# Kernel tuning notes

Hardware: AMD Instinct MI355X
Metric: run time of the kernel (lower is better)

Reference implementation:

```python
import jax, jax.numpy as jnp
import numpy as np

B, V, T, K, N = 2048, 256, 11, 8, 8
H = 2 ** N - 1  # 255 combination neurons per slot


def setup_inputs() -> dict:
    key = jax.random.key(0)
    k0, k1, k2, k3, k4 = jax.random.split(key, 5)
    # one-hot character ids, matching make_scanner_batch semantics: (B, V, T, K)
    ids = jax.random.randint(k0, (B, T, K), 0, V)
    x_unfolded = jax.nn.one_hot(ids, V, axis=1, dtype=jnp.float32)
    # scanner_w ~ U(-1/sqrt(V), 1/sqrt(V)), shape (N, V, K)
    bv = 1.0 / np.sqrt(V).astype(np.float32)
    scanner_w = jax.random.uniform(k1, (N, V, K), jnp.float32, -bv, bv)
    # grouped 1x1 conv: torch weight (K*H, N, 1) -> store (K*H, N); fan_in = N
    bh = 1.0 / np.sqrt(N).astype(np.float32)
    hidden_w = jax.random.uniform(k2, (K * H, N), jnp.float32, -bh, bh)
    # output 1x1 conv: (2, K*H, 1) -> (2, K*H); fan_in = K*H
    bo = 1.0 / np.sqrt(K * H).astype(np.float32)
    out_w = jax.random.uniform(k3, (2, K * H), jnp.float32, -bo, bo)
    out_b = jax.random.uniform(k4, (2,), jnp.float32, -bo, bo)
    return {"x_unfolded": x_unfolded, "scanner_w": scanner_w,
            "hidden_w": hidden_w, "out_w": out_w, "out_b": out_b}


def reference(x_unfolded, scanner_w, hidden_w, out_w, out_b):
    # x_unfolded: (B, V, T, K); scanner_w: (N, V, K)
    b, v, t, k = x_unfolded.shape
    n = scanner_w.shape[0]
    h_per_slot = hidden_w.shape[0] // k
    # one-hot matmul (equivalent to a gather): result (B, K, N, T),
    # i.e. channel order after reshape is slot-major (k*N + n), matching
    # torch's permute(0,3,1,2).reshape(B, K*N, T).
    h = jax.nn.relu(jnp.einsum('bvtk,nvk->bknt', x_unfolded, scanner_w))
    # grouped 1x1 conv with groups=K: group k maps its N scanner values to
    # h_per_slot neurons. torch weight (K*H, N, 1) -> (K, H, N), where output
    # channel o belongs to group o // H.
    hw = hidden_w.reshape(k, h_per_slot, n)
    h2 = jax.nn.relu(jnp.einsum('bknt,khn->bkht', h, hw)).reshape(b, k * h_per_slot, t)
    # final 1x1 conv with bias: (B, 2, T)
    return jnp.einsum('bct,oc->bot', h2, out_w) + out_b[None, :, None]
```

## Files before the change

kernel.cpp:

```cpp
#include <hip/hip_runtime.h>

constexpr int B_ = 2048;
constexpr int V_ = 256;
constexpr int T_ = 11;
constexpr int K_ = 8;
constexpr int N_ = 8;
constexpr int H_ = 255;
constexpr int TK = T_ * K_;
constexpr int XB = V_ * TK;
constexpr int SLAB = 92;

__global__ __launch_bounds__(256, 3)
void scanner_fused(const float* __restrict__ x,
                   const float* __restrict__ sw,
                   const float* __restrict__ hw,
                   const float* __restrict__ ow,
                   const float* __restrict__ ob,
                   float* __restrict__ out)
{
    __shared__ int   ids_sh[TK];
    __shared__ float hsh[K_ * SLAB];
    __shared__ float wred[4][22];

    const int tid = threadIdx.x;
    const int b   = blockIdx.x;

    const float4* xb = (const float4*)(x + (size_t)b * XB);
    #pragma unroll
    for (int c = 0; c < 3; ++c) {
        const int nload = (c < 2) ? 8 : 6;
        float4 vbuf[8];
        #pragma unroll
        for (int i = 0; i < 8; ++i)
            if (i < nload) vbuf[i] = xb[(c * 8 + i) * 256 + tid];
        #pragma unroll
        for (int i = 0; i < 8; ++i) {
            if (i < nload) {
                const float4 q = vbuf[i];
                if ((q.x + q.y) + (q.z + q.w) != 0.0f) {
                    const int F = ((c * 8 + i) * 256 + tid) * 4;
                    if (q.x != 0.0f) { const int f = F;     const int v = f / TK; ids_sh[f - v * TK] = v; }
                    if (q.y != 0.0f) { const int f = F + 1; const int v = f / TK; ids_sh[f - v * TK] = v; }
                    if (q.z != 0.0f) { const int f = F + 2; const int v = f / TK; ids_sh[f - v * TK] = v; }
                    if (q.w != 0.0f) { const int f = F + 3; const int v = f / TK; ids_sh[f - v * TK] = v; }
                }
            }
        }
    }
    __syncthreads();

    #pragma unroll
    for (int j = 0; j < 3; ++j) {
        const int idx = j * 256 + tid;
        if (idx < TK * N_) {
            const int entry = idx >> 3;
            const int n     = idx & 7;
            const int t     = entry >> 3;
            const int k     = entry & 7;
            const int v     = ids_sh[entry];
            hsh[k * SLAB + t * 8 + n] = fmaxf(sw[(n * V_ + v) * K_ + k], 0.0f);
        }
    }
    __syncthreads();

    const int k2 = tid >> 5;
    const int hb = tid & 31;

    float hreg[T_][N_];
    #pragma unroll
    for (int t = 0; t < T_; ++t) {
        const float4* p = (const float4*)(hsh + k2 * SLAB + t * 8);
        const float4 a0 = p[0];
        const float4 a1 = p[1];
        hreg[t][0] = a0.x; hreg[t][1] = a0.y; hreg[t][2] = a0.z; hreg[t][3] = a0.w;
        hreg[t][4] = a1.x; hreg[t][5] = a1.y; hreg[t][6] = a1.z; hreg[t][7] = a1.w;
    }

    float acc0[T_], acc1[T_];
    #pragma unroll
    for (int t = 0; t < T_; ++t) { acc0[t] = 0.0f; acc1[t] = 0.0f; }

    #pragma unroll
    for (int i = 0; i < 8; ++i) {
        const int hh = hb + 32 * i;
        if (hh < H_) {
            const int row = k2 * H_ + hh;
            const float4* hwp = (const float4*)(hw + row * 8);
            const float4 w0 = hwp[0];
            const float4 w1 = hwp[1];
            const float o0 = ow[row];
            const float o1 = ow[K_ * H_ + row];
            #pragma unroll
            for (int t = 0; t < T_; ++t) {
                float pre = w0.x * hreg[t][0];
                pre = fmaf(w0.y, hreg[t][1], pre);
                pre = fmaf(w0.z, hreg[t][2], pre);
                pre = fmaf(w0.w, hreg[t][3], pre);
                pre = fmaf(w1.x, hreg[t][4], pre);
                pre = fmaf(w1.y, hreg[t][5], pre);
                pre = fmaf(w1.z, hreg[t][6], pre);
                pre = fmaf(w1.w, hreg[t][7], pre);
                const float h2 = fmaxf(pre, 0.0f);
                acc0[t] = fmaf(h2, o0, acc0[t]);
                acc1[t] = fmaf(h2, o1, acc1[t]);
            }
        }
    }

    #pragma unroll
    for (int t = 0; t < T_; ++t) {
        #pragma unroll
        for (int off = 32; off >= 1; off >>= 1) {
            acc0[t] += __shfl_xor(acc0[t], off, 64);
            acc1[t] += __shfl_xor(acc1[t], off, 64);
        }
    }
    const int wave = tid >> 6;
    const int lane = tid & 63;
    if (lane == 0) {
        #pragma unroll
        for (int t = 0; t < T_; ++t) {
            wred[wave][t]      = acc0[t];
            wred[wave][11 + t] = acc1[t];
        }
    }
    __syncthreads();

    if (tid < 22) {
        const float s = wred[0][tid] + wred[1][tid] + wred[2][tid] + wred[3][tid];
        out[(size_t)b * 22 + tid] = s + ob[tid / 11];
    }
}

extern "C" void kernel_launch(void* const* d_in, const int* in_sizes, int n_in,
                              void* d_out, int out_size, void* d_ws, size_t ws_size,
                              hipStream_t stream) {
    const float* x  = (const float*)d_in[0];
    const float* sw = (const float*)d_in[1];
    const float* hw = (const float*)d_in[2];
    const float* ow = (const float*)d_in[3];
    const float* ob = (const float*)d_in[4];
    float* out = (float*)d_out;

    scanner_fused<<<B_, 256, 0, stream>>>(x, sw, hw, ow, ob, out);
}
```

Before: 271.7 us.

## Split one-hot id scan into separate kernel feeding MLP kernel via workspace

Un-fuses the kernel. A bandwidth-bound scan kernel decodes the one-hot input into integer ids and writes them to workspace. A second compute kernel reads those ids and runs the scanner gather plus the two MLP layers. The aim is to let each phase run with occupancy suited to it (the scan kernel allows 4 blocks per SM) and to keep the 93 MB streaming read from competing with the FMA-heavy MLP. The costs are an extra launch, a global round trip for the ids, and the loss of overlap between memory and compute inside a single block.

```diff
diff --git a/kernel.cpp b/kernel.cpp
--- a/kernel.cpp
+++ b/kernel.cpp
@@ -10,13 +10,45 @@
 constexpr int XB = V_ * TK;
 constexpr int SLAB = 92;
 
+__global__ __launch_bounds__(256, 4)
+void scan_ids(const float* __restrict__ x,
+              int* __restrict__ ids)
+{
+    const int tid = threadIdx.x;
+    const int b   = blockIdx.x;
+    const uint4* xb = (const uint4*)(x + (size_t)b * XB);
+    int* __restrict__ idb = ids + b * TK;
+
+    #pragma unroll
+    for (int c = 0; c < 3; ++c) {
+        const int nload = (c < 2) ? 8 : 6;
+        uint4 vbuf[8];
+        #pragma unroll
+        for (int i = 0; i < 8; ++i)
+            if (i < nload) vbuf[i] = xb[(c * 8 + i) * 256 + tid];
+        #pragma unroll
+        for (int i = 0; i < 8; ++i) {
+            if (i < nload) {
+                const uint4 q = vbuf[i];
+                if (q.x | q.y | q.z | q.w) {
+                    const int F = ((c * 8 + i) * 256 + tid) * 4;
+                    if (q.x) { const int f = F;     const int v = f / TK; idb[f - v * TK] = v; }
+                    if (q.y) { const int f = F + 1; const int v = f / TK; idb[f - v * TK] = v; }
+                    if (q.z) { const int f = F + 2; const int v = f / TK; idb[f - v * TK] = v; }
+                    if (q.w) { const int f = F + 3; const int v = f / TK; idb[f - v * TK] = v; }
+                }
+            }
+        }
+    }
+}
+
 __global__ __launch_bounds__(256, 3)
-void scanner_fused(const float* __restrict__ x,
-                   const float* __restrict__ sw,
-                   const float* __restrict__ hw,
-                   const float* __restrict__ ow,
-                   const float* __restrict__ ob,
-                   float* __restrict__ out)
+void scanner_mlp(const int* __restrict__ ids,
+                 const float* __restrict__ sw,
+                 const float* __restrict__ hw,
+                 const float* __restrict__ ow,
+                 const float* __restrict__ ob,
+                 float* __restrict__ out)
 {
     __shared__ int   ids_sh[TK];
     __shared__ float hsh[K_ * SLAB];
@@ -25,28 +57,7 @@
     const int tid = threadIdx.x;
     const int b   = blockIdx.x;
 
-    const float4* xb = (const float4*)(x + (size_t)b * XB);
-    #pragma unroll
-    for (int c = 0; c < 3; ++c) {
-        const int nload = (c < 2) ? 8 : 6;
-        float4 vbuf[8];
-        #pragma unroll
-        for (int i = 0; i < 8; ++i)
-            if (i < nload) vbuf[i] = xb[(c * 8 + i) * 256 + tid];
-        #pragma unroll
-        for (int i = 0; i < 8; ++i) {
-            if (i < nload) {
-                const float4 q = vbuf[i];
-                if ((q.x + q.y) + (q.z + q.w) != 0.0f) {
-                    const int F = ((c * 8 + i) * 256 + tid) * 4;
-                    if (q.x != 0.0f) { const int f = F;     const int v = f / TK; ids_sh[f - v * TK] = v; }
-                    if (q.y != 0.0f) { const int f = F + 1; const int v = f / TK; ids_sh[f - v * TK] = v; }
-                    if (q.z != 0.0f) { const int f = F + 2; const int v = f / TK; ids_sh[f - v * TK] = v; }
-                    if (q.w != 0.0f) { const int f = F + 3; const int v = f / TK; ids_sh[f - v * TK] = v; }
-                }
-            }
-        }
-    }
+    if (tid < TK) ids_sh[tid] = ids[b * TK + tid];
     __syncthreads();
 
     #pragma unroll
@@ -142,5 +153,8 @@
     const float* ob = (const float*)d_in[4];
     float* out = (float*)d_out;
 
-    scanner_fused<<<B_, 256, 0, stream>>>(x, sw, hw, ow, ob, out);
+    int* ids = (int*)d_ws;
+
+    scan_ids<<<B_, 256, 0, stream>>>(x, ids);
+    scanner_mlp<<<B_, 256, 0, stream>>>(ids, sw, hw, ow, ob, out);
 }
```

After: 282.8 us. 4.1% more time.
